# Kernel tuning notes

Hardware: AMD Instinct MI355X
Metric: run time of the kernel (lower is better)

## Reference

```python
import jax, jax.numpy as jnp
import numpy as np

N_NODES = 50000
N_EDGES = 600000
IN_DIM = 128
HID = 64
HEADS = 4
OUT_DIM = 64
EPS = 1e-5


def setup_inputs() -> dict:
    key = jax.random.key(0)
    ks = jax.random.split(key, 20)
    s = 0.05
    inp = {
        "x": jax.random.normal(ks[0], (N_NODES, IN_DIM), jnp.float32),
        "edge_index": jax.random.randint(ks[1], (2, N_EDGES), 0, N_NODES, jnp.int32),
        "drift_weight": jax.random.uniform(ks[2], (1,), jnp.float32),
        # GAT layer 1: in_dim -> heads*hid, concat
        "W1": jax.random.normal(ks[3], (IN_DIM, HEADS * HID), jnp.float32) * s,
        "a_src1": jax.random.normal(ks[4], (HEADS, HID), jnp.float32) * s,
        "a_dst1": jax.random.normal(ks[5], (HEADS, HID), jnp.float32) * s,
        "b1": jnp.zeros((HEADS * HID,), jnp.float32),
        # BatchNorm over heads*hid features
        "gamma": jnp.ones((HEADS * HID,), jnp.float32),
        "beta": jnp.zeros((HEADS * HID,), jnp.float32),
        # GAT layer 2: heads*hid -> hid, mean over heads
        "W2": jax.random.normal(ks[6], (HEADS * HID, HEADS * HID), jnp.float32) * s,
        "a_src2": jax.random.normal(ks[7], (HEADS, HID), jnp.float32) * s,
        "a_dst2": jax.random.normal(ks[8], (HEADS, HID), jnp.float32) * s,
        "b2": jnp.zeros((HID,), jnp.float32),
        # GCN layers
        "Wg1": jax.random.normal(ks[9], (IN_DIM, HID), jnp.float32) * s,
        "bg1": jnp.zeros((HID,), jnp.float32),
        "Wg2": jax.random.normal(ks[10], (HID, OUT_DIM), jnp.float32) * s,
        "bg2": jnp.zeros((OUT_DIM,), jnp.float32),
    }
    return inp


def _gat_layer(x, src, dst, W, a_src, a_dst, b, concat):
    # PyG GATConv (dropout disabled at eval): h = xW; e_ij = LeakyReLU(a_src.h_j + a_dst.h_i)
    # softmax over incoming edges of each dst node; out_i = sum_j alpha_ij h_j
    n = x.shape[0]
    H, C = a_src.shape
    h = (x @ W).reshape(n, H, C)                      # [N,H,C]
    e = jax.nn.leaky_relu(
        (h * a_src).sum(-1)[src] + (h * a_dst).sum(-1)[dst], 0.2
    )                                                 # [E,H]
    m = jax.ops.segment_max(e, dst, num_segments=n)
    p = jnp.exp(e - m[dst])
    z = jax.ops.segment_sum(p, dst, num_segments=n)
    alpha = p / z[dst]                                # [E,H]
    out = jax.ops.segment_sum(h[src] * alpha[:, :, None], dst, num_segments=n)
    out = out.reshape(n, H * C) if concat else out.mean(axis=1)
    return out + b


def _gcn_layer(x, src, dst, W, b):
    n = x.shape[0]
    deg = jax.ops.segment_sum(jnp.ones(src.shape[0], x.dtype), dst, num_segments=n)
    dinv = jax.lax.rsqrt(jnp.maximum(deg, 1.0))
    h = x @ W
    norm = (dinv[src] * dinv[dst])[:, None]           # [E,1]
    return jax.ops.segment_sum(h[src] * norm, dst, num_segments=n) + b


def _batchnorm(x, gamma, beta):
    mu = x.mean(axis=0)
    var = x.var(axis=0)
    return (x - mu) * jax.lax.rsqrt(var + EPS) * gamma + beta


def reference(x, edge_index, drift_weight, W1, a_src1, a_dst1, b1, gamma, beta,
              W2, a_src2, a_dst2, b2, Wg1, bg1, Wg2, bg2):
    n = x.shape[0]
    loop = jnp.arange(n, dtype=edge_index.dtype)
    src = jnp.concatenate([edge_index[0], loop])
    dst = jnp.concatenate([edge_index[1], loop])

    # GAT branch
    h = _gat_layer(x, src, dst, W1, a_src1, a_dst1, b1, concat=True)
    h = jax.nn.elu(_batchnorm(h, gamma, beta))
    h_gat = _gat_layer(h, src, dst, W2, a_src2, a_dst2, b2, concat=False)  # [N,HID]

    # GCN branch
    g = jax.nn.relu(_gcn_layer(x, src, dst, Wg1, bg1))
    h_gcn = _gcn_layer(g, src, dst, Wg2, bg2)                              # [N,OUT]

    # drift-weighted fusion
    w = drift_weight[0]
    return w * h_gat + (1.0 - w) * h_gcn
```

## Files before the change

kernel.cpp:

```cpp
#include <hip/hip_runtime.h>

#define N_NODES 50000
#define M_PAD   50048
#define N_EDGES 600000
#define ETOT    650000
#define EPS     1e-5f
#define SCAN_BLOCKS 196

typedef short bf16x8 __attribute__((ext_vector_type(8)));
typedef float f32x4  __attribute__((ext_vector_type(4)));

static __device__ __forceinline__ float leaky(float v) { return v >= 0.f ? v : 0.2f * v; }

static __device__ __forceinline__ ushort f2bf(float f) {
  unsigned u = __float_as_uint(f);
  return (ushort)((u + 0x7fff + ((u >> 16) & 1)) >> 16);
}
static __device__ __forceinline__ float bf2f(ushort u) {
  return __uint_as_float(((unsigned)u) << 16);
}

template <int K, bool OUTBF, bool PERM>
__global__ __launch_bounds__(256) void gemm_bf16(
    const ushort* __restrict__ A, const ushort* __restrict__ Bt,
    void* __restrict__ C, int M, int Nfull) {
  __shared__ char As[64 * 128];
  __shared__ char Bs[64 * 128];
  const int tid = threadIdx.x;
  const int w = tid >> 6, lane = tid & 63;
  const int wr = w >> 1, wc = w & 1;
  const int m0 = blockIdx.x * 64, n0 = blockIdx.y * 64;

  f32x4 acc[2][2] = {};

  for (int k0 = 0; k0 < K; k0 += 64) {
    __syncthreads();
#pragma unroll
    for (int j = 0; j < 2; ++j) {
      int i = tid + j * 256;
      int row = i >> 3;
      int cb = (i & 7) * 16;
      int dst = row * 128 + (cb ^ ((row & 7) << 4));
      uint4 va = *(const uint4*)((const char*)A + ((size_t)(m0 + row) * K + k0) * 2 + cb);
      *(uint4*)(As + dst) = va;
      uint4 vb = *(const uint4*)((const char*)Bt + ((size_t)(n0 + row) * K + k0) * 2 + cb);
      *(uint4*)(Bs + dst) = vb;
    }
    __syncthreads();
#pragma unroll
    for (int c = 0; c < 2; ++c) {
      bf16x8 af[2], bfr[2];
      int kb = (lane >> 4) * 16 + c * 64;
#pragma unroll
      for (int m = 0; m < 2; ++m) {
        int lr = wr * 32 + m * 16 + (lane & 15);
        af[m] = *(const bf16x8*)(As + lr * 128 + (kb ^ ((lr & 7) << 4)));
      }
#pragma unroll
      for (int n = 0; n < 2; ++n) {
        int lr = wc * 32 + n * 16 + (lane & 15);
        bfr[n] = *(const bf16x8*)(Bs + lr * 128 + (kb ^ ((lr & 7) << 4)));
      }
#pragma unroll
      for (int m = 0; m < 2; ++m)
#pragma unroll
        for (int n = 0; n < 2; ++n)
          acc[m][n] = __builtin_amdgcn_mfma_f32_16x16x32_bf16(af[m], bfr[n], acc[m][n], 0, 0, 0);
    }
  }
#pragma unroll
  for (int m = 0; m < 2; ++m)
#pragma unroll
    for (int n = 0; n < 2; ++n)
#pragma unroll
      for (int i = 0; i < 4; ++i) {
        int row = m0 + wr * 32 + m * 16 + (lane >> 4) * 4 + i;
        int col = n0 + wc * 32 + n * 16 + (lane & 15);
        if (row < M) {
          if (OUTBF) {
            int oc = PERM ? (((col & 63) << 2) | (col >> 6)) : col;
            ((ushort*)C)[(size_t)row * Nfull + oc] = f2bf(acc[m][n][i]);
          } else {
            ((float*)C)[(size_t)row * Nfull + col] = acc[m][n][i];
          }
        }
      }
}

__global__ __launch_bounds__(256) void cast_x_bf16(const float* __restrict__ x, ushort* __restrict__ o) {
  int i = blockIdx.x * 256 + threadIdx.x;
  if (i >= M_PAD * 32) return;
  int i4 = i * 4;
  int row = i4 >> 7;
  ushort4 r;
  if (row < N_NODES) {
    const float4 v = *(const float4*)(x + i4);
    r.x = f2bf(v.x); r.y = f2bf(v.y); r.z = f2bf(v.z); r.w = f2bf(v.w);
  } else {
    r.x = r.y = r.z = r.w = 0;
  }
  *(ushort4*)(o + i4) = r;
}

__global__ __launch_bounds__(256) void tcast_w(const float* __restrict__ W, ushort* __restrict__ Wt,
                                               int K, int N) {
  int i = blockIdx.x * 256 + threadIdx.x;
  if (i >= K * N) return;
  int k = i / N, n = i - k * N;
  Wt[n * K + k] = f2bf(W[i]);
}

__global__ __launch_bounds__(256) void attn_scores_bf(
    const ushort* __restrict__ h, const float* __restrict__ a_src,
    const float* __restrict__ a_dst, float* __restrict__ ssrc, float* __restrict__ sdst) {
  const int wave = threadIdx.x >> 6, lane = threadIdx.x & 63;
  const int row = blockIdx.x * 4 + wave;
  if (row >= N_NODES) return;
  const ushort4 hv = *(const ushort4*)(h + (size_t)row * 256 + lane * 4);
  float h0 = bf2f(hv.x), h1 = bf2f(hv.y), h2 = bf2f(hv.z), h3 = bf2f(hv.w);
  const float4 as = *(const float4*)(a_src + lane * 4);
  const float4 ad = *(const float4*)(a_dst + lane * 4);
  float ps = h0 * as.x + h1 * as.y + h2 * as.z + h3 * as.w;
  float pd = h0 * ad.x + h1 * ad.y + h2 * ad.z + h3 * ad.w;
#pragma unroll
  for (int off = 1; off < 16; off <<= 1) {
    ps += __shfl_xor(ps, off);
    pd += __shfl_xor(pd, off);
  }
  if ((lane & 15) == 0) {
    int hh = lane >> 4;
    ssrc[row * 4 + hh] = ps;
    sdst[row * 4 + hh] = pd;
  }
}

__global__ __launch_bounds__(256) void attn_scores_perm(
    const ushort* __restrict__ hp, const float* __restrict__ a_src,
    const float* __restrict__ a_dst, float* __restrict__ ssrc, float* __restrict__ sdst) {
  const int wave = threadIdx.x >> 6, lane = threadIdx.x & 63;
  const int row = blockIdx.x * 4 + wave;
  if (row >= N_NODES) return;
  const ushort4 hv = *(const ushort4*)(hp + (size_t)row * 256 + lane * 4);
  float h0 = bf2f(hv.x), h1 = bf2f(hv.y), h2 = bf2f(hv.z), h3 = bf2f(hv.w);
  float s0 = h0 * a_src[lane],       d0 = h0 * a_dst[lane];
  float s1 = h1 * a_src[64 + lane],  d1 = h1 * a_dst[64 + lane];
  float s2 = h2 * a_src[128 + lane], d2 = h2 * a_dst[128 + lane];
  float s3 = h3 * a_src[192 + lane], d3 = h3 * a_dst[192 + lane];
#pragma unroll
  for (int off = 1; off < 64; off <<= 1) {
    s0 += __shfl_xor(s0, off); d0 += __shfl_xor(d0, off);
    s1 += __shfl_xor(s1, off); d1 += __shfl_xor(d1, off);
    s2 += __shfl_xor(s2, off); d2 += __shfl_xor(d2, off);
    s3 += __shfl_xor(s3, off); d3 += __shfl_xor(d3, off);
  }
  if (lane == 0) {
    float4 sv = { s0, s1, s2, s3 };
    float4 dv = { d0, d1, d2, d3 };
    *(float4*)(ssrc + row * 4) = sv;
    *(float4*)(sdst + row * 4) = dv;
  }
}

static __device__ __forceinline__ void edge_sd(const int* ei, int e, int& src, int& dst) {
  if (e < N_EDGES) { src = ei[e]; dst = ei[N_EDGES + e]; }
  else             { src = dst = e - N_EDGES; }
}

__global__ __launch_bounds__(256) void deg_count_int(const int* __restrict__ ei, int* __restrict__ degi) {
  int e = blockIdx.x * 256 + threadIdx.x;
  if (e >= ETOT) return;
  int dst = (e < N_EDGES) ? ei[N_EDGES + e] : (e - N_EDGES);
  atomicAdd(&degi[dst], 1);
}

__global__ __launch_bounds__(256) void scan1(const int* __restrict__ degi,
                                             int* __restrict__ partial, int* __restrict__ bsum) {
  __shared__ int sm[256];
  int i = blockIdx.x * 256 + threadIdx.x;
  int v = (i < N_NODES) ? degi[i] : 0;
  sm[threadIdx.x] = v;
  __syncthreads();
#pragma unroll
  for (int off = 1; off < 256; off <<= 1) {
    int t = (threadIdx.x >= off) ? sm[threadIdx.x - off] : 0;
    __syncthreads();
    sm[threadIdx.x] += t;
    __syncthreads();
  }
  if (i < N_NODES) partial[i] = sm[threadIdx.x] - v;
  if (threadIdx.x == 255) bsum[blockIdx.x] = sm[255];
}

__global__ __launch_bounds__(256) void scan2(int* __restrict__ bsum) {
  __shared__ int sm[256];
  int v = (threadIdx.x < SCAN_BLOCKS) ? bsum[threadIdx.x] : 0;
  sm[threadIdx.x] = v;
  __syncthreads();
#pragma unroll
  for (int off = 1; off < 256; off <<= 1) {
    int t = (threadIdx.x >= off) ? sm[threadIdx.x - off] : 0;
    __syncthreads();
    sm[threadIdx.x] += t;
    __syncthreads();
  }
  if (threadIdx.x < SCAN_BLOCKS) bsum[threadIdx.x] = sm[threadIdx.x] - v;
}

__global__ __launch_bounds__(256) void scan3(int* __restrict__ rowstart, const int* __restrict__ bsum,
                                             int* __restrict__ cursor, const int* __restrict__ degi,
                                             float* __restrict__ dinv) {
  int i = blockIdx.x * 256 + threadIdx.x;
  if (i >= N_NODES) return;
  int r = rowstart[i] + bsum[blockIdx.x];
  rowstart[i] = r;
  cursor[i] = r;
  dinv[i] = rsqrtf(fmaxf((float)degi[i], 1.0f));
}

__global__ __launch_bounds__(256) void scatter_k(const int* __restrict__ ei,
                                                 int* __restrict__ cursor, int* __restrict__ csr,
                                                 int* __restrict__ csrd) {
  int e = blockIdx.x * 256 + threadIdx.x;
  if (e >= ETOT) return;
  int src, dst; edge_sd(ei, e, src, dst);
  int pos = atomicAdd(&cursor[dst], 1);
  csr[pos] = src;
  csrd[pos] = dst;
}

__global__ __launch_bounds__(256) void edge_p(
    const int* __restrict__ csr, const int* __restrict__ csrd,
    const float* __restrict__ ssrc, const float* __restrict__ sdst,
    float* __restrict__ pcsr) {
  int e = blockIdx.x * 256 + threadIdx.x;
  if (e >= ETOT) return;
  int src = csr[e], dst = csrd[e];
  const float4 ss = *(const float4*)(ssrc + src * 4);
  const float4 sd = *(const float4*)(sdst + dst * 4);
  float4 p;
  p.x = __expf(leaky(ss.x + sd.x));
  p.y = __expf(leaky(ss.y + sd.y));
  p.z = __expf(leaky(ss.z + sd.z));
  p.w = __expf(leaky(ss.w + sd.w));
  *(float4*)(pcsr + (size_t)e * 4) = p;
}

__global__ __launch_bounds__(256) void gat_agg1_bf(
    const int* __restrict__ rowstart, const int* __restrict__ degi, const int* __restrict__ csr,
    const float* __restrict__ pcsr, const ushort* __restrict__ h, float* __restrict__ outp) {
  int dst = blockIdx.x * 4 + (threadIdx.x >> 6);
  if (dst >= N_NODES) return;
  int lane = threadIdx.x & 63;
  int hh = lane >> 4;
  int rs = rowstart[dst], re = rs + degi[dst];
  float z = 0.f;
  float ax = 0.f, ay = 0.f, az = 0.f, aw = 0.f;
  int j = rs;
  for (; j + 1 < re; j += 2) {
    int s0 = csr[j], s1 = csr[j + 1];
    float p0 = pcsr[(size_t)j * 4 + hh];
    float p1 = pcsr[(size_t)(j + 1) * 4 + hh];
    const ushort4 hv0 = *(const ushort4*)(h + (size_t)s0 * 256 + lane * 4);
    const ushort4 hv1 = *(const ushort4*)(h + (size_t)s1 * 256 + lane * 4);
    z += p0 + p1;
    ax += p0 * bf2f(hv0.x) + p1 * bf2f(hv1.x);
    ay += p0 * bf2f(hv0.y) + p1 * bf2f(hv1.y);
    az += p0 * bf2f(hv0.z) + p1 * bf2f(hv1.z);
    aw += p0 * bf2f(hv0.w) + p1 * bf2f(hv1.w);
  }
  if (j < re) {
    int s0 = csr[j];
    float p0 = pcsr[(size_t)j * 4 + hh];
    const ushort4 hv0 = *(const ushort4*)(h + (size_t)s0 * 256 + lane * 4);
    z += p0;
    ax += p0 * bf2f(hv0.x); ay += p0 * bf2f(hv0.y);
    az += p0 * bf2f(hv0.z); aw += p0 * bf2f(hv0.w);
  }
  float inv = 1.f / z;
  float4 o = { ax * inv, ay * inv, az * inv, aw * inv };
  *(float4*)(outp + (size_t)dst * 256 + lane * 4) = o;
}

__global__ __launch_bounds__(256) void gat_agg2_perm(
    const int* __restrict__ rowstart, const int* __restrict__ degi, const int* __restrict__ csr,
    const float* __restrict__ pcsr, const ushort* __restrict__ hp, float* __restrict__ outp) {
  int dst = blockIdx.x * 4 + (threadIdx.x >> 6);
  if (dst >= N_NODES) return;
  int lane = threadIdx.x & 63;
  int rs = rowstart[dst], re = rs + degi[dst];
  float z0 = 0.f, z1 = 0.f, z2 = 0.f, z3 = 0.f;
  float a0 = 0.f, a1 = 0.f, a2 = 0.f, a3 = 0.f;
  int j = rs;
  for (; j + 1 < re; j += 2) {
    int s0 = csr[j], s1 = csr[j + 1];
    const float4 p0 = *(const float4*)(pcsr + (size_t)j * 4);
    const float4 p1 = *(const float4*)(pcsr + (size_t)(j + 1) * 4);
    const ushort4 hv0 = *(const ushort4*)(hp + (size_t)s0 * 256 + lane * 4);
    const ushort4 hv1 = *(const ushort4*)(hp + (size_t)s1 * 256 + lane * 4);
    z0 += p0.x + p1.x; z1 += p0.y + p1.y; z2 += p0.z + p1.z; z3 += p0.w + p1.w;
    a0 += p0.x * bf2f(hv0.x) + p1.x * bf2f(hv1.x);
    a1 += p0.y * bf2f(hv0.y) + p1.y * bf2f(hv1.y);
    a2 += p0.z * bf2f(hv0.z) + p1.z * bf2f(hv1.z);
    a3 += p0.w * bf2f(hv0.w) + p1.w * bf2f(hv1.w);
  }
  if (j < re) {
    int s0 = csr[j];
    const float4 p0 = *(const float4*)(pcsr + (size_t)j * 4);
    const ushort4 hv0 = *(const ushort4*)(hp + (size_t)s0 * 256 + lane * 4);
    z0 += p0.x; z1 += p0.y; z2 += p0.z; z3 += p0.w;
    a0 += p0.x * bf2f(hv0.x); a1 += p0.y * bf2f(hv0.y);
    a2 += p0.z * bf2f(hv0.z); a3 += p0.w * bf2f(hv0.w);
  }
  outp[(size_t)dst * 64 + lane] = 0.25f * (a0 / z0 + a1 / z1 + a2 / z2 + a3 / z3);
}

__global__ __launch_bounds__(256) void gcn_agg_relu_bf(
    const int* __restrict__ rowstart, const int* __restrict__ degi, const int* __restrict__ csr,
    const ushort* __restrict__ g, const float* __restrict__ dinv, const float* __restrict__ bias,
    ushort* __restrict__ outp) {
  int dst = blockIdx.x * 4 + (threadIdx.x >> 6);
  if (dst >= N_NODES) return;
  int lane = threadIdx.x & 63;
  int rs = rowstart[dst], re = rs + degi[dst];
  float acc = 0.f;
  int j = rs;
  for (; j + 1 < re; j += 2) {
    int s0 = csr[j], s1 = csr[j + 1];
    float d0 = dinv[s0], d1 = dinv[s1];
    float v0 = bf2f(g[(size_t)s0 * 64 + lane]);
    float v1 = bf2f(g[(size_t)s1 * 64 + lane]);
    acc += d0 * v0 + d1 * v1;
  }
  if (j < re) {
    int s0 = csr[j];
    acc += dinv[s0] * bf2f(g[(size_t)s0 * 64 + lane]);
  }
  float v = acc * dinv[dst] + bias[lane];
  outp[(size_t)dst * 64 + lane] = f2bf(fmaxf(v, 0.f));
}

__global__ __launch_bounds__(256) void gcn_agg_fuse_bf(
    const int* __restrict__ rowstart, const int* __restrict__ degi, const int* __restrict__ csr,
    const ushort* __restrict__ g2, const float* __restrict__ dinv, const float* __restrict__ bg2,
    const float* __restrict__ hgat, const float* __restrict__ b2, const float* __restrict__ dw,
    float* __restrict__ outp) {
  int dst = blockIdx.x * 4 + (threadIdx.x >> 6);
  if (dst >= N_NODES) return;
  int lane = threadIdx.x & 63;
  int rs = rowstart[dst], re = rs + degi[dst];
  float acc = 0.f;
  int j = rs;
  for (; j + 1 < re; j += 2) {
    int s0 = csr[j], s1 = csr[j + 1];
    float d0 = dinv[s0], d1 = dinv[s1];
    float v0 = bf2f(g2[(size_t)s0 * 64 + lane]);
    float v1 = bf2f(g2[(size_t)s1 * 64 + lane]);
    acc += d0 * v0 + d1 * v1;
  }
  if (j < re) {
    int s0 = csr[j];
    acc += dinv[s0] * bf2f(g2[(size_t)s0 * 64 + lane]);
  }
  float w = dw[0];
  float gcn = acc * dinv[dst] + bg2[lane];
  float gat = hgat[(size_t)dst * 64 + lane] + b2[lane];
  outp[(size_t)dst * 64 + lane] = w * gat + (1.f - w) * gcn;
}

__global__ __launch_bounds__(256) void bn_stats(
    const float* __restrict__ x, float* __restrict__ sum, float* __restrict__ sumsq) {
  int f = threadIdx.x;
  int r0 = blockIdx.x * 64;
  int rend = min(r0 + 64, N_NODES);
  float s = 0.f, s2 = 0.f;
  for (int r = r0; r < rend; ++r) {
    float v = x[(size_t)r * 256 + f];
    s += v; s2 += v * v;
  }
  atomicAdd(&sum[f], s);
  atomicAdd(&sumsq[f], s2);
}

__global__ __launch_bounds__(256) void bn_apply_bf16(
    const float* __restrict__ x, const float* __restrict__ sum, const float* __restrict__ sumsq,
    const float* __restrict__ gamma, const float* __restrict__ beta, ushort* __restrict__ o) {
  size_t i = (size_t)blockIdx.x * 256 + threadIdx.x;
  if (i >= (size_t)N_NODES * 256) return;
  int f = (int)(i & 255);
  const float invN = 1.0f / N_NODES;
  float mu = sum[f] * invN;
  float var = sumsq[f] * invN - mu * mu;
  float v = (x[i] - mu) * rsqrtf(var + EPS) * gamma[f] + beta[f];
  float e = v > 0.f ? v : expf(v) - 1.0f;
  o[i] = f2bf(e);
}

extern "C" void kernel_launch(void* const* d_in, const int* in_sizes, int n_in,
                              void* d_out, int out_size, void* d_ws, size_t ws_size,
                              hipStream_t stream) {
  const float* x     = (const float*)d_in[0];
  const int*   ei    = (const int*)d_in[1];
  const float* dw    = (const float*)d_in[2];
  const float* W1    = (const float*)d_in[3];
  const float* as1   = (const float*)d_in[4];
  const float* ad1   = (const float*)d_in[5];
  const float* gamma = (const float*)d_in[7];
  const float* beta  = (const float*)d_in[8];
  const float* W2    = (const float*)d_in[9];
  const float* as2   = (const float*)d_in[10];
  const float* ad2   = (const float*)d_in[11];
  const float* b2    = (const float*)d_in[12];
  const float* Wg1   = (const float*)d_in[13];
  const float* bg1   = (const float*)d_in[14];
  const float* Wg2   = (const float*)d_in[15];
  const float* bg2   = (const float*)d_in[16];
  float* out = (float*)d_out;

  char* p = (char*)d_ws;
  size_t off = 0;
  auto alloc = [&](size_t bytes) {
    char* r = p + off;
    off = (off + bytes + 255) & ~(size_t)255;
    return r;
  };
  float*  bufB  = (float*)alloc((size_t)N_NODES * 256 * 4);
  float*  bufC  = (float*)alloc((size_t)N_NODES * 64 * 4);
  ushort* xbf   = (ushort*)alloc((size_t)M_PAD * 128 * 2);
  ushort* R1    = (ushort*)alloc((size_t)M_PAD * 256 * 2);
  ushort* g1bf  = (ushort*)alloc((size_t)N_NODES * 64 * 2);
  ushort* gbf   = (ushort*)alloc((size_t)M_PAD * 64 * 2);
  ushort* g2bf  = (ushort*)alloc((size_t)N_NODES * 64 * 2);
  ushort* w1t   = (ushort*)alloc((size_t)256 * 128 * 2);
  ushort* w2t   = (ushort*)alloc((size_t)256 * 256 * 2);
  ushort* wg1t  = (ushort*)alloc((size_t)64 * 128 * 2);
  ushort* wg2t  = (ushort*)alloc((size_t)64 * 64 * 2);
  float*  ssrc1 = (float*)alloc((size_t)N_NODES * 4 * 4);
  float*  sdst1 = (float*)alloc((size_t)N_NODES * 4 * 4);
  float*  ssrc2 = (float*)alloc((size_t)N_NODES * 4 * 4);
  float*  sdst2 = (float*)alloc((size_t)N_NODES * 4 * 4);
  int*    degi  = (int*)alloc((size_t)N_NODES * 4);
  int*    rowst = (int*)alloc((size_t)N_NODES * 4);
  int*    cursor= (int*)alloc((size_t)N_NODES * 4);
  int*    bsum  = (int*)alloc(SCAN_BLOCKS * 4);
  float*  dinv  = (float*)alloc((size_t)N_NODES * 4);
  int*    csr   = (int*)alloc((size_t)ETOT * 4);
  int*    csrd  = (int*)alloc((size_t)ETOT * 4);
  float*  pcsr  = (float*)alloc((size_t)ETOT * 4 * 4);
  float*  bnsum = (float*)alloc(256 * 4);
  float*  bnsq  = (float*)alloc(256 * 4);
  ushort* h2p   = (ushort*)bufB;

  const dim3 blk(256);
  const int egrid = (ETOT + 255) / 256;
  const int ngrid = 12500;

  hipMemsetAsync(degi, 0, (size_t)N_NODES * 4, stream);
  hipMemsetAsync(bnsum, 0, 256 * 4, stream);
  hipMemsetAsync(bnsq, 0, 256 * 4, stream);
  hipMemsetAsync(R1 + (size_t)N_NODES * 256, 0, (size_t)(M_PAD - N_NODES) * 256 * 2, stream);
  hipMemsetAsync(gbf + (size_t)N_NODES * 64, 0, (size_t)(M_PAD - N_NODES) * 64 * 2, stream);

  deg_count_int<<<egrid, blk, 0, stream>>>(ei, degi);
  scan1<<<SCAN_BLOCKS, blk, 0, stream>>>(degi, rowst, bsum);
  scan2<<<1, blk, 0, stream>>>(bsum);
  scan3<<<SCAN_BLOCKS, blk, 0, stream>>>(rowst, bsum, cursor, degi, dinv);
  scatter_k<<<egrid, blk, 0, stream>>>(ei, cursor, csr, csrd);
  cast_x_bf16<<<(M_PAD * 32 + 255) / 256, blk, 0, stream>>>(x, xbf);
  tcast_w<<<(128 * 256 + 255) / 256, blk, 0, stream>>>(W1, w1t, 128, 256);
  tcast_w<<<(256 * 256 + 255) / 256, blk, 0, stream>>>(W2, w2t, 256, 256);
  tcast_w<<<(128 * 64 + 255) / 256, blk, 0, stream>>>(Wg1, wg1t, 128, 64);
  tcast_w<<<(64 * 64 + 255) / 256, blk, 0, stream>>>(Wg2, wg2t, 64, 64);

  gemm_bf16<128, true, false><<<dim3(782, 4), blk, 0, stream>>>(xbf, w1t, R1, N_NODES, 256);
  gemm_bf16<128, true, false><<<dim3(782, 1), blk, 0, stream>>>(xbf, wg1t, g1bf, N_NODES, 64);

  attn_scores_bf<<<ngrid, blk, 0, stream>>>(R1, as1, ad1, ssrc1, sdst1);
  edge_p<<<egrid, blk, 0, stream>>>(csr, csrd, ssrc1, sdst1, pcsr);
  gat_agg1_bf<<<ngrid, blk, 0, stream>>>(rowst, degi, csr, pcsr, R1, bufB);

  gcn_agg_relu_bf<<<ngrid, blk, 0, stream>>>(rowst, degi, csr, g1bf, dinv, bg1, gbf);
  gemm_bf16<64, true, false><<<dim3(782, 1), blk, 0, stream>>>(gbf, wg2t, g2bf, N_NODES, 64);

  bn_stats<<<(N_NODES + 63) / 64, blk, 0, stream>>>(bufB, bnsum, bnsq);
  bn_apply_bf16<<<(int)(((size_t)N_NODES * 256 + 255) / 256), blk, 0, stream>>>(
      bufB, bnsum, bnsq, gamma, beta, R1);

  gemm_bf16<256, true, true><<<dim3(782, 4), blk, 0, stream>>>(R1, w2t, h2p, N_NODES, 256);
  attn_scores_perm<<<ngrid, blk, 0, stream>>>(h2p, as2, ad2, ssrc2, sdst2);
  edge_p<<<egrid, blk, 0, stream>>>(csr, csrd, ssrc2, sdst2, pcsr);
  gat_agg2_perm<<<ngrid, blk, 0, stream>>>(rowst, degi, csr, pcsr, h2p, bufC);

  gcn_agg_fuse_bf<<<ngrid, blk, 0, stream>>>(rowst, degi, csr, g2bf, dinv, bg2, bufC, b2, dw, out);
}
```

Before: 567.4 us.

## Store GAT layer-1 aggregate in bf16, unroll gathers by four, merge prep kernels

New measurement: 495.3 us. 12.7% less time.

```diff
diff --git a/kernel.cpp b/kernel.cpp
--- a/kernel.cpp
+++ b/kernel.cpp
@@ -102,12 +102,40 @@
   *(ushort4*)(o + i4) = r;
 }
 
-__global__ __launch_bounds__(256) void tcast_w(const float* __restrict__ W, ushort* __restrict__ Wt,
-                                               int K, int N) {
-  int i = blockIdx.x * 256 + threadIdx.x;
-  if (i >= K * N) return;
-  int k = i / N, n = i - k * N;
-  Wt[n * K + k] = f2bf(W[i]);
+__global__ __launch_bounds__(256) void prep_small(
+    const float* __restrict__ W1, const float* __restrict__ W2,
+    const float* __restrict__ Wg1, const float* __restrict__ Wg2,
+    ushort* __restrict__ w1t, ushort* __restrict__ w2t,
+    ushort* __restrict__ wg1t, ushort* __restrict__ wg2t,
+    ushort* __restrict__ r1pad, ushort* __restrict__ aggpad, ushort* __restrict__ gpad) {
+  int bid = blockIdx.x, t = threadIdx.x;
+  ushort4 zz; zz.x = zz.y = zz.z = zz.w = 0;
+  if (bid < 12) {
+    int i = bid * 256 + t;
+    *(ushort4*)(r1pad + i * 4) = zz;
+  } else if (bid < 24) {
+    int i = (bid - 12) * 256 + t;
+    *(ushort4*)(aggpad + i * 4) = zz;
+  } else if (bid < 27) {
+    int i = (bid - 24) * 256 + t;
+    if (i < 768) *(ushort4*)(gpad + i * 4) = zz;
+  } else if (bid < 155) {
+    int i = (bid - 27) * 256 + t;
+    int k = i >> 8, n = i & 255;
+    w1t[n * 128 + k] = f2bf(W1[i]);
+  } else if (bid < 411) {
+    int i = (bid - 155) * 256 + t;
+    int k = i >> 8, n = i & 255;
+    w2t[n * 256 + k] = f2bf(W2[i]);
+  } else if (bid < 443) {
+    int i = (bid - 411) * 256 + t;
+    int k = i >> 6, n = i & 63;
+    wg1t[n * 128 + k] = f2bf(Wg1[i]);
+  } else {
+    int i = (bid - 443) * 256 + t;
+    int k = i >> 6, n = i & 63;
+    wg2t[n * 64 + k] = f2bf(Wg2[i]);
+  }
 }
 
 __global__ __launch_bounds__(256) void attn_scores_bf(
@@ -247,7 +275,7 @@
 
 __global__ __launch_bounds__(256) void gat_agg1_bf(
     const int* __restrict__ rowstart, const int* __restrict__ degi, const int* __restrict__ csr,
-    const float* __restrict__ pcsr, const ushort* __restrict__ h, float* __restrict__ outp) {
+    const float* __restrict__ pcsr, const ushort* __restrict__ h, ushort* __restrict__ outp) {
   int dst = blockIdx.x * 4 + (threadIdx.x >> 6);
   if (dst >= N_NODES) return;
   int lane = threadIdx.x & 63;
@@ -256,29 +284,35 @@
   float z = 0.f;
   float ax = 0.f, ay = 0.f, az = 0.f, aw = 0.f;
   int j = rs;
-  for (; j + 1 < re; j += 2) {
-    int s0 = csr[j], s1 = csr[j + 1];
+  for (; j + 3 < re; j += 4) {
+    int s0 = csr[j], s1 = csr[j + 1], s2 = csr[j + 2], s3 = csr[j + 3];
     float p0 = pcsr[(size_t)j * 4 + hh];
     float p1 = pcsr[(size_t)(j + 1) * 4 + hh];
-    const ushort4 hv0 = *(const ushort4*)(h + (size_t)s0 * 256 + lane * 4);
-    const ushort4 hv1 = *(const ushort4*)(h + (size_t)s1 * 256 + lane * 4);
-    z += p0 + p1;
-    ax += p0 * bf2f(hv0.x) + p1 * bf2f(hv1.x);
-    ay += p0 * bf2f(hv0.y) + p1 * bf2f(hv1.y);
-    az += p0 * bf2f(hv0.z) + p1 * bf2f(hv1.z);
-    aw += p0 * bf2f(hv0.w) + p1 * bf2f(hv1.w);
-  }
-  if (j < re) {
+    float p2 = pcsr[(size_t)(j + 2) * 4 + hh];
+    float p3 = pcsr[(size_t)(j + 3) * 4 + hh];
+    const ushort4 v0 = *(const ushort4*)(h + (size_t)s0 * 256 + lane * 4);
+    const ushort4 v1 = *(const ushort4*)(h + (size_t)s1 * 256 + lane * 4);
+    const ushort4 v2 = *(const ushort4*)(h + (size_t)s2 * 256 + lane * 4);
+    const ushort4 v3 = *(const ushort4*)(h + (size_t)s3 * 256 + lane * 4);
+    z += (p0 + p1) + (p2 + p3);
+    ax += p0 * bf2f(v0.x) + p1 * bf2f(v1.x) + p2 * bf2f(v2.x) + p3 * bf2f(v3.x);
+    ay += p0 * bf2f(v0.y) + p1 * bf2f(v1.y) + p2 * bf2f(v2.y) + p3 * bf2f(v3.y);
+    az += p0 * bf2f(v0.z) + p1 * bf2f(v1.z) + p2 * bf2f(v2.z) + p3 * bf2f(v3.z);
+    aw += p0 * bf2f(v0.w) + p1 * bf2f(v1.w) + p2 * bf2f(v2.w) + p3 * bf2f(v3.w);
+  }
+  for (; j < re; ++j) {
     int s0 = csr[j];
     float p0 = pcsr[(size_t)j * 4 + hh];
-    const ushort4 hv0 = *(const ushort4*)(h + (size_t)s0 * 256 + lane * 4);
+    const ushort4 v0 = *(const ushort4*)(h + (size_t)s0 * 256 + lane * 4);
     z += p0;
-    ax += p0 * bf2f(hv0.x); ay += p0 * bf2f(hv0.y);
-    az += p0 * bf2f(hv0.z); aw += p0 * bf2f(hv0.w);
+    ax += p0 * bf2f(v0.x); ay += p0 * bf2f(v0.y);
+    az += p0 * bf2f(v0.z); aw += p0 * bf2f(v0.w);
   }
   float inv = 1.f / z;
-  float4 o = { ax * inv, ay * inv, az * inv, aw * inv };
-  *(float4*)(outp + (size_t)dst * 256 + lane * 4) = o;
+  ushort4 o;
+  o.x = f2bf(ax * inv); o.y = f2bf(ay * inv);
+  o.z = f2bf(az * inv); o.w = f2bf(aw * inv);
+  *(ushort4*)(outp + (size_t)dst * 256 + lane * 4) = o;
 }
 
 __global__ __launch_bounds__(256) void gat_agg2_perm(
@@ -291,25 +325,32 @@
   float z0 = 0.f, z1 = 0.f, z2 = 0.f, z3 = 0.f;
   float a0 = 0.f, a1 = 0.f, a2 = 0.f, a3 = 0.f;
   int j = rs;
-  for (; j + 1 < re; j += 2) {
-    int s0 = csr[j], s1 = csr[j + 1];
+  for (; j + 3 < re; j += 4) {
+    int s0 = csr[j], s1 = csr[j + 1], s2 = csr[j + 2], s3 = csr[j + 3];
     const float4 p0 = *(const float4*)(pcsr + (size_t)j * 4);
     const float4 p1 = *(const float4*)(pcsr + (size_t)(j + 1) * 4);
-    const ushort4 hv0 = *(const ushort4*)(hp + (size_t)s0 * 256 + lane * 4);
-    const ushort4 hv1 = *(const ushort4*)(hp + (size_t)s1 * 256 + lane * 4);
-    z0 += p0.x + p1.x; z1 += p0.y + p1.y; z2 += p0.z + p1.z; z3 += p0.w + p1.w;
-    a0 += p0.x * bf2f(hv0.x) + p1.x * bf2f(hv1.x);
-    a1 += p0.y * bf2f(hv0.y) + p1.y * bf2f(hv1.y);
-    a2 += p0.z * bf2f(hv0.z) + p1.z * bf2f(hv1.z);
-    a3 += p0.w * bf2f(hv0.w) + p1.w * bf2f(hv1.w);
-  }
-  if (j < re) {
+    const float4 p2 = *(const float4*)(pcsr + (size_t)(j + 2) * 4);
+    const float4 p3 = *(const float4*)(pcsr + (size_t)(j + 3) * 4);
+    const ushort4 v0 = *(const ushort4*)(hp + (size_t)s0 * 256 + lane * 4);
+    const ushort4 v1 = *(const ushort4*)(hp + (size_t)s1 * 256 + lane * 4);
+    const ushort4 v2 = *(const ushort4*)(hp + (size_t)s2 * 256 + lane * 4);
+    const ushort4 v3 = *(const ushort4*)(hp + (size_t)s3 * 256 + lane * 4);
+    z0 += (p0.x + p1.x) + (p2.x + p3.x);
+    z1 += (p0.y + p1.y) + (p2.y + p3.y);
+    z2 += (p0.z + p1.z) + (p2.z + p3.z);
+    z3 += (p0.w + p1.w) + (p2.w + p3.w);
+    a0 += p0.x * bf2f(v0.x) + p1.x * bf2f(v1.x) + p2.x * bf2f(v2.x) + p3.x * bf2f(v3.x);
+    a1 += p0.y * bf2f(v0.y) + p1.y * bf2f(v1.y) + p2.y * bf2f(v2.y) + p3.y * bf2f(v3.y);
+    a2 += p0.z * bf2f(v0.z) + p1.z * bf2f(v1.z) + p2.z * bf2f(v2.z) + p3.z * bf2f(v3.z);
+    a3 += p0.w * bf2f(v0.w) + p1.w * bf2f(v1.w) + p2.w * bf2f(v2.w) + p3.w * bf2f(v3.w);
+  }
+  for (; j < re; ++j) {
     int s0 = csr[j];
     const float4 p0 = *(const float4*)(pcsr + (size_t)j * 4);
-    const ushort4 hv0 = *(const ushort4*)(hp + (size_t)s0 * 256 + lane * 4);
+    const ushort4 v0 = *(const ushort4*)(hp + (size_t)s0 * 256 + lane * 4);
     z0 += p0.x; z1 += p0.y; z2 += p0.z; z3 += p0.w;
-    a0 += p0.x * bf2f(hv0.x); a1 += p0.y * bf2f(hv0.y);
-    a2 += p0.z * bf2f(hv0.z); a3 += p0.w * bf2f(hv0.w);
+    a0 += p0.x * bf2f(v0.x); a1 += p0.y * bf2f(v0.y);
+    a2 += p0.z * bf2f(v0.z); a3 += p0.w * bf2f(v0.w);
   }
   outp[(size_t)dst * 64 + lane] = 0.25f * (a0 / z0 + a1 / z1 + a2 / z2 + a3 / z3);
 }
@@ -324,14 +365,16 @@
   int rs = rowstart[dst], re = rs + degi[dst];
   float acc = 0.f;
   int j = rs;
-  for (; j + 1 < re; j += 2) {
-    int s0 = csr[j], s1 = csr[j + 1];
-    float d0 = dinv[s0], d1 = dinv[s1];
+  for (; j + 3 < re; j += 4) {
+    int s0 = csr[j], s1 = csr[j + 1], s2 = csr[j + 2], s3 = csr[j + 3];
+    float d0 = dinv[s0], d1 = dinv[s1], d2 = dinv[s2], d3 = dinv[s3];
     float v0 = bf2f(g[(size_t)s0 * 64 + lane]);
     float v1 = bf2f(g[(size_t)s1 * 64 + lane]);
-    acc += d0 * v0 + d1 * v1;
-  }
-  if (j < re) {
+    float v2 = bf2f(g[(size_t)s2 * 64 + lane]);
+    float v3 = bf2f(g[(size_t)s3 * 64 + lane]);
+    acc += (d0 * v0 + d1 * v1) + (d2 * v2 + d3 * v3);
+  }
+  for (; j < re; ++j) {
     int s0 = csr[j];
     acc += dinv[s0] * bf2f(g[(size_t)s0 * 64 + lane]);
   }
@@ -350,14 +393,16 @@
   int rs = rowstart[dst], re = rs + degi[dst];
   float acc = 0.f;
   int j = rs;
-  for (; j + 1 < re; j += 2) {
-    int s0 = csr[j], s1 = csr[j + 1];
-    float d0 = dinv[s0], d1 = dinv[s1];
+  for (; j + 3 < re; j += 4) {
+    int s0 = csr[j], s1 = csr[j + 1], s2 = csr[j + 2], s3 = csr[j + 3];
+    float d0 = dinv[s0], d1 = dinv[s1], d2 = dinv[s2], d3 = dinv[s3];
     float v0 = bf2f(g2[(size_t)s0 * 64 + lane]);
     float v1 = bf2f(g2[(size_t)s1 * 64 + lane]);
-    acc += d0 * v0 + d1 * v1;
-  }
-  if (j < re) {
+    float v2 = bf2f(g2[(size_t)s2 * 64 + lane]);
+    float v3 = bf2f(g2[(size_t)s3 * 64 + lane]);
+    acc += (d0 * v0 + d1 * v1) + (d2 * v2 + d3 * v3);
+  }
+  for (; j < re; ++j) {
     int s0 = csr[j];
     acc += dinv[s0] * bf2f(g2[(size_t)s0 * 64 + lane]);
   }
@@ -367,32 +412,48 @@
   outp[(size_t)dst * 64 + lane] = w * gat + (1.f - w) * gcn;
 }
 
-__global__ __launch_bounds__(256) void bn_stats(
-    const float* __restrict__ x, float* __restrict__ sum, float* __restrict__ sumsq) {
+__global__ __launch_bounds__(256) void bn_stats_bf(
+    const ushort* __restrict__ x, float* __restrict__ sum, float* __restrict__ sumsq) {
   int f = threadIdx.x;
   int r0 = blockIdx.x * 64;
   int rend = min(r0 + 64, N_NODES);
   float s = 0.f, s2 = 0.f;
   for (int r = r0; r < rend; ++r) {
-    float v = x[(size_t)r * 256 + f];
+    float v = bf2f(x[(size_t)r * 256 + f]);
     s += v; s2 += v * v;
   }
   atomicAdd(&sum[f], s);
   atomicAdd(&sumsq[f], s2);
 }
 
-__global__ __launch_bounds__(256) void bn_apply_bf16(
-    const float* __restrict__ x, const float* __restrict__ sum, const float* __restrict__ sumsq,
-    const float* __restrict__ gamma, const float* __restrict__ beta, ushort* __restrict__ o) {
-  size_t i = (size_t)blockIdx.x * 256 + threadIdx.x;
-  if (i >= (size_t)N_NODES * 256) return;
-  int f = (int)(i & 255);
+__global__ __launch_bounds__(256) void bn_apply_bf(
+    ushort* __restrict__ x, const float* __restrict__ sum, const float* __restrict__ sumsq,
+    const float* __restrict__ gamma, const float* __restrict__ beta) {
+  int i = blockIdx.x * 256 + threadIdx.x;
+  if (i >= N_NODES * 64) return;
+  int i4 = i * 4;
+  int f0 = i4 & 255;
   const float invN = 1.0f / N_NODES;
-  float mu = sum[f] * invN;
-  float var = sumsq[f] * invN - mu * mu;
-  float v = (x[i] - mu) * rsqrtf(var + EPS) * gamma[f] + beta[f];
-  float e = v > 0.f ? v : expf(v) - 1.0f;
-  o[i] = f2bf(e);
+  const float4 sm = *(const float4*)(sum + f0);
+  const float4 sq = *(const float4*)(sumsq + f0);
+  const float4 gm = *(const float4*)(gamma + f0);
+  const float4 bt = *(const float4*)(beta + f0);
+  ushort4 v = *(ushort4*)(x + i4);
+  float mu, var, t;
+  ushort4 o;
+  mu = sm.x * invN; var = sq.x * invN - mu * mu;
+  t = (bf2f(v.x) - mu) * rsqrtf(var + EPS) * gm.x + bt.x;
+  o.x = f2bf(t > 0.f ? t : expf(t) - 1.0f);
+  mu = sm.y * invN; var = sq.y * invN - mu * mu;
+  t = (bf2f(v.y) - mu) * rsqrtf(var + EPS) * gm.y + bt.y;
+  o.y = f2bf(t > 0.f ? t : expf(t) - 1.0f);
+  mu = sm.z * invN; var = sq.z * invN - mu * mu;
+  t = (bf2f(v.z) - mu) * rsqrtf(var + EPS) * gm.z + bt.z;
+  o.z = f2bf(t > 0.f ? t : expf(t) - 1.0f);
+  mu = sm.w * invN; var = sq.w * invN - mu * mu;
+  t = (bf2f(v.w) - mu) * rsqrtf(var + EPS) * gm.w + bt.w;
+  o.w = f2bf(t > 0.f ? t : expf(t) - 1.0f);
+  *(ushort4*)(x + i4) = o;
 }
 
 extern "C" void kernel_launch(void* const* d_in, const int* in_sizes, int n_in,
@@ -423,7 +484,8 @@
     off = (off + bytes + 255) & ~(size_t)255;
     return r;
   };
-  float*  bufB  = (float*)alloc((size_t)N_NODES * 256 * 4);
+  ushort* aggbf = (ushort*)alloc((size_t)M_PAD * 256 * 2);
+  ushort* h2p   = (ushort*)alloc((size_t)N_NODES * 256 * 2);
   float*  bufC  = (float*)alloc((size_t)N_NODES * 64 * 4);
   ushort* xbf   = (ushort*)alloc((size_t)M_PAD * 128 * 2);
   ushort* R1    = (ushort*)alloc((size_t)M_PAD * 256 * 2);
@@ -438,7 +500,10 @@
   float*  sdst1 = (float*)alloc((size_t)N_NODES * 4 * 4);
   float*  ssrc2 = (float*)alloc((size_t)N_NODES * 4 * 4);
   float*  sdst2 = (float*)alloc((size_t)N_NODES * 4 * 4);
-  int*    degi  = (int*)alloc((size_t)N_NODES * 4);
+  char*   zr    = alloc((size_t)N_NODES * 4 + 512 * 4);
+  int*    degi  = (int*)zr;
+  float*  bnsum = (float*)(zr + (size_t)N_NODES * 4);
+  float*  bnsq  = bnsum + 256;
   int*    rowst = (int*)alloc((size_t)N_NODES * 4);
   int*    cursor= (int*)alloc((size_t)N_NODES * 4);
   int*    bsum  = (int*)alloc(SCAN_BLOCKS * 4);
@@ -446,46 +511,39 @@
   int*    csr   = (int*)alloc((size_t)ETOT * 4);
   int*    csrd  = (int*)alloc((size_t)ETOT * 4);
   float*  pcsr  = (float*)alloc((size_t)ETOT * 4 * 4);
-  float*  bnsum = (float*)alloc(256 * 4);
-  float*  bnsq  = (float*)alloc(256 * 4);
-  ushort* h2p   = (ushort*)bufB;
 
   const dim3 blk(256);
   const int egrid = (ETOT + 255) / 256;
   const int ngrid = 12500;
 
-  hipMemsetAsync(degi, 0, (size_t)N_NODES * 4, stream);
-  hipMemsetAsync(bnsum, 0, 256 * 4, stream);
-  hipMemsetAsync(bnsq, 0, 256 * 4, stream);
-  hipMemsetAsync(R1 + (size_t)N_NODES * 256, 0, (size_t)(M_PAD - N_NODES) * 256 * 2, stream);
-  hipMemsetAsync(gbf + (size_t)N_NODES * 64, 0, (size_t)(M_PAD - N_NODES) * 64 * 2, stream);
+  hipMemsetAsync(zr, 0, (size_t)N_NODES * 4 + 512 * 4, stream);
+
+  prep_small<<<459, blk, 0, stream>>>(W1, W2, Wg1, Wg2, w1t, w2t, wg1t, wg2t,
+                                      R1 + (size_t)N_NODES * 256,
+                                      aggbf + (size_t)N_NODES * 256,
+                                      gbf + (size_t)N_NODES * 64);
+  cast_x_bf16<<<(M_PAD * 32 + 255) / 256, blk, 0, stream>>>(x, xbf);
 
   deg_count_int<<<egrid, blk, 0, stream>>>(ei, degi);
   scan1<<<SCAN_BLOCKS, blk, 0, stream>>>(degi, rowst, bsum);
   scan2<<<1, blk, 0, stream>>>(bsum);
   scan3<<<SCAN_BLOCKS, blk, 0, stream>>>(rowst, bsum, cursor, degi, dinv);
   scatter_k<<<egrid, blk, 0, stream>>>(ei, cursor, csr, csrd);
-  cast_x_bf16<<<(M_PAD * 32 + 255) / 256, blk, 0, stream>>>(x, xbf);
-  tcast_w<<<(128 * 256 + 255) / 256, blk, 0, stream>>>(W1, w1t, 128, 256);
-  tcast_w<<<(256 * 256 + 255) / 256, blk, 0, stream>>>(W2, w2t, 256, 256);
-  tcast_w<<<(128 * 64 + 255) / 256, blk, 0, stream>>>(Wg1, wg1t, 128, 64);
-  tcast_w<<<(64 * 64 + 255) / 256, blk, 0, stream>>>(Wg2, wg2t, 64, 64);
 
   gemm_bf16<128, true, false><<<dim3(782, 4), blk, 0, stream>>>(xbf, w1t, R1, N_NODES, 256);
   gemm_bf16<128, true, false><<<dim3(782, 1), blk, 0, stream>>>(xbf, wg1t, g1bf, N_NODES, 64);
 
   attn_scores_bf<<<ngrid, blk, 0, stream>>>(R1, as1, ad1, ssrc1, sdst1);
   edge_p<<<egrid, blk, 0, stream>>>(csr, csrd, ssrc1, sdst1, pcsr);
-  gat_agg1_bf<<<ngrid, blk, 0, stream>>>(rowst, degi, csr, pcsr, R1, bufB);
+  gat_agg1_bf<<<ngrid, blk, 0, stream>>>(rowst, degi, csr, pcsr, R1, aggbf);
 
   gcn_agg_relu_bf<<<ngrid, blk, 0, stream>>>(rowst, degi, csr, g1bf, dinv, bg1, gbf);
   gemm_bf16<64, true, false><<<dim3(782, 1), blk, 0, stream>>>(gbf, wg2t, g2bf, N_NODES, 64);
 
-  bn_stats<<<(N_NODES + 63) / 64, blk, 0, stream>>>(bufB, bnsum, bnsq);
-  bn_apply_bf16<<<(int)(((size_t)N_NODES * 256 + 255) / 256), blk, 0, stream>>>(
-      bufB, bnsum, bnsq, gamma, beta, R1);
-
-  gemm_bf16<256, true, true><<<dim3(782, 4), blk, 0, stream>>>(R1, w2t, h2p, N_NODES, 256);
+  bn_stats_bf<<<(N_NODES + 63) / 64, blk, 0, stream>>>(aggbf, bnsum, bnsq);
+  bn_apply_bf<<<(N_NODES * 64 + 255) / 256, blk, 0, stream>>>(aggbf, bnsum, bnsq, gamma, beta);
+
+  gemm_bf16<256, true, true><<<dim3(782, 4), blk, 0, stream>>>(aggbf, w2t, h2p, N_NODES, 256);
   attn_scores_perm<<<ngrid, blk, 0, stream>>>(h2p, as2, ad2, ssrc2, sdst2);
   edge_p<<<egrid, blk, 0, stream>>>(csr, csrd, ssrc2, sdst2, pcsr);
   gat_agg2_perm<<<ngrid, blk, 0, stream>>>(rowst, degi, csr, pcsr, h2p, bufC);
```
